# Kernel tuning notes

Measured on AMD Instinct MI355X. Metric: run time of the kernel, lower is better.

Reference implementation:

```python
import jax, jax.numpy as jnp
import numpy as np

D_MODEL = 1024
D_INNER = 4096   # expand=4
D_STATE = 16
D_CONV = 4
DT_RANK = 64     # ceil(d_model/16)
BATCH = 2
SEQLEN = 2048


def setup_inputs() -> dict:
    key = jax.random.key(0)
    ks = jax.random.split(key, 9)
    s = 0.02
    x = jax.random.normal(ks[0], (BATCH, SEQLEN, D_MODEL), jnp.float32)
    in_proj_w = jax.random.normal(ks[1], (D_MODEL, 2 * D_INNER), jnp.float32) * s
    conv_w = jax.random.normal(ks[2], (D_INNER, D_CONV), jnp.float32) * 0.3
    conv_b = jax.random.normal(ks[3], (D_INNER,), jnp.float32) * 0.02
    x_proj_w = jax.random.normal(ks[4], (D_INNER, DT_RANK + 2 * D_STATE), jnp.float32) * s
    dt_proj_w = jax.random.normal(ks[5], (DT_RANK, D_INNER), jnp.float32) * (DT_RANK ** -0.5)
    dt_proj_b = jax.random.normal(ks[6], (D_INNER,), jnp.float32) * 0.1 - 4.0  # small softplus(dt)
    # A = repeat(arange(1, d_state+1)) as in mamba-ssm; A_log = log(A)
    A_log = jnp.log(jnp.broadcast_to(jnp.arange(1, D_STATE + 1, dtype=jnp.float32), (D_INNER, D_STATE)))
    D = jnp.ones((D_INNER,), jnp.float32)
    out_proj_w = jax.random.normal(ks[7], (D_INNER, D_MODEL), jnp.float32) * s
    return {"x": x, "in_proj_w": in_proj_w, "conv_w": conv_w, "conv_b": conv_b,
            "x_proj_w": x_proj_w, "dt_proj_w": dt_proj_w, "dt_proj_b": dt_proj_b,
            "A_log": A_log, "D": D, "out_proj_w": out_proj_w}


def reference(x, in_proj_w, conv_w, conv_b, x_proj_w, dt_proj_w, dt_proj_b, A_log, D, out_proj_w):
    Bsz, L, _ = x.shape
    # input projection -> (x branch, gate z), each [B, L, d_inner]
    xz = x @ in_proj_w
    xc, z = jnp.split(xz, 2, axis=-1)
    # causal depthwise conv1d, kernel D_CONV, left-padded
    xp = jnp.pad(xc, ((0, 0), (D_CONV - 1, 0), (0, 0)))
    xconv = conv_b + sum(xp[:, k:k + L, :] * conv_w[:, k] for k in range(D_CONV))
    xs = jax.nn.silu(xconv)  # [B, L, d_inner]
    # input-dependent SSM params
    proj = xs @ x_proj_w  # [B, L, dt_rank + 2*d_state]
    dt_lo, Bt, Ct = jnp.split(proj, [DT_RANK, DT_RANK + D_STATE], axis=-1)
    dt = jax.nn.softplus(dt_lo @ dt_proj_w + dt_proj_b)  # [B, L, d_inner]
    A = -jnp.exp(A_log)  # [d_inner, d_state]

    def step(h, inp):
        dt_t, B_t, C_t, u_t = inp  # [B,dI], [B,dS], [B,dS], [B,dI]
        dA = jnp.exp(dt_t[..., None] * A)                       # [B, dI, dS]
        h = h * dA + (dt_t * u_t)[..., None] * B_t[:, None, :]  # [B, dI, dS]
        y = jnp.einsum('bdn,bn->bd', h, C_t)                    # [B, dI]
        return h, y

    h0 = jnp.zeros((Bsz, D_INNER, D_STATE), x.dtype)
    inps = (dt.transpose(1, 0, 2), Bt.transpose(1, 0, 2),
            Ct.transpose(1, 0, 2), xs.transpose(1, 0, 2))
    _, ys = jax.lax.scan(step, h0, inps)  # ys: [L, B, d_inner]
    y = ys.transpose(1, 0, 2) + xs * D
    y = y * jax.nn.silu(z)
    return y @ out_proj_w
```

## Files before the change

### kernel.cpp

```cpp
#include <hip/hip_runtime.h>
#include <hip/hip_bf16.h>

#define D_MODEL 1024
#define D_INNER 4096
#define D_STATE 16
#define D_CONV 4
#define DT_RANK 64
#define BATCH 2
#define SEQLEN 2048
#define MROWS (BATCH * SEQLEN)
#define NPROJ (DT_RANK + 2 * D_STATE)
#define PST 128
#define NC 32
#define TC (SEQLEN / NC)
#define KSPLIT 8
#define KSP6 4

typedef unsigned short u16;
typedef unsigned int u32;
typedef __attribute__((ext_vector_type(8))) short short8;
typedef __attribute__((ext_vector_type(4))) float floatx4;

#define LOG2E 1.44269504089f

__device__ __forceinline__ float bf2f(u16 u) {
    union { u32 i; float f; } v; v.i = ((u32)u) << 16; return v.f;
}
__device__ __forceinline__ u16 f2bf(float f) {
    union { float f; u32 i; } v; v.f = f;
    u32 x = v.i;
    u32 r = x + 0x7fffu + ((x >> 16) & 1u);
    return (u16)(r >> 16);
}
__device__ __forceinline__ float softplus_fast(float x) {
    float l = __logf(1.f + __expf(-fabsf(x)));
    return x > 0.f ? x + l : l;
}
__device__ __forceinline__ float sigmoid_fast(float x) {
    return __builtin_amdgcn_rcpf(1.f + __expf(-x));
}
__device__ __forceinline__ float exp2_hw(float x) {
    float r;
    asm("v_exp_f32 %0, %1" : "=v"(r) : "v"(x));
    return r;
}
__device__ __forceinline__ void pow_tree16(float r, float* pw) {
    pw[0] = r;
    pw[1] = r * r;
    pw[2] = pw[1] * r;
    pw[3] = pw[1] * pw[1];
    pw[4] = pw[3] * r;
    pw[5] = pw[3] * pw[1];
    pw[6] = pw[3] * pw[2];
    pw[7] = pw[3] * pw[3];
#pragma unroll
    for (int k = 0; k < 8; k++) pw[8 + k] = pw[7] * pw[k];
}
__device__ __forceinline__ void async_cp16(const u16* g, u16* l) {
    __builtin_amdgcn_global_load_lds((const __attribute__((address_space(1))) void*)g,
                                     (__attribute__((address_space(3))) void*)l, 16, 0, 0);
}

__global__ __launch_bounds__(256) void detect_dtype(const u16* __restrict__ x, int* __restrict__ flag,
                                                    int* __restrict__ sflag) {
    __shared__ int cnt;
    if (threadIdx.x == 0) { cnt = 0; *sflag = 0; }
    __syncthreads();
    int local = 0;
    for (int k = 0; k < 16; k++) {
        int e = threadIdx.x * 8192 + k * 512;
        u16 v = x[2 * e];
        int ex = (v >> 7) & 0xFF;
        if (ex >= 0x68 && ex <= 0x8F) local++;
    }
    atomicAdd(&cnt, local);
    __syncthreads();
    if (threadIdx.x == 0) *flag = (cnt >= 2458) ? 1 : 0;
}

__global__ __launch_bounds__(256) void ingest16(const void* __restrict__ src, u16* __restrict__ dst,
                                                int n, const int* __restrict__ flag) {
    int i = blockIdx.x * 256 + threadIdx.x;
    if (i >= n) return;
    if (*flag) dst[i] = ((const u16*)src)[i];
    else       dst[i] = f2bf(((const float*)src)[i]);
}

__global__ __launch_bounds__(256) void prep_small(const void* __restrict__ cw, const void* __restrict__ cb,
                                                  const void* __restrict__ dtb, const void* __restrict__ Dv,
                                                  const void* __restrict__ Alog,
                                                  u16* __restrict__ cw16, u16* __restrict__ cb16,
                                                  u16* __restrict__ dtb16, u16* __restrict__ D16,
                                                  float* __restrict__ A, const int* __restrict__ flag,
                                                  int* __restrict__ sflag) {
    int i = blockIdx.x * 256 + threadIdx.x;
    int isb = *flag;
    if (i < D_INNER * D_CONV)
        cw16[i] = isb ? ((const u16*)cw)[i] : f2bf(((const float*)cw)[i]);
    if (i < D_INNER) {
        cb16[i]  = isb ? ((const u16*)cb)[i]  : f2bf(((const float*)cb)[i]);
        dtb16[i] = isb ? ((const u16*)dtb)[i] : f2bf(((const float*)dtb)[i]);
        D16[i]   = isb ? ((const u16*)Dv)[i]  : f2bf(((const float*)Dv)[i]);
    }
    if (i < D_INNER * D_STATE) {
        float v = isb ? bf2f(((const u16*)Alog)[i]) : ((const float*)Alog)[i];
        float a = -expf(v);
        A[i] = a;
        float tgt = (float)((i & 15) + 1);
        if (fabsf(a + tgt) > 4e-6f * tgt) atomicOr(sflag, 1);
    }
}

__global__ __launch_bounds__(256) void transpose_w(const void* __restrict__ W, u16* __restrict__ WT,
                                                   int K, int N, const int* __restrict__ flag) {
    __shared__ float t[32][33];
    int k0 = blockIdx.y * 32, n0 = blockIdx.x * 32;
    int tid = threadIdx.x;
    int r = tid >> 3, c4 = (tid & 7) * 4;
    int isb = *flag;
    size_t base = (size_t)(k0 + r) * N + n0 + c4;
    float4 v;
    if (isb) { ushort4 u4 = *(const ushort4*)((const u16*)W + base);
               v = make_float4(bf2f(u4.x), bf2f(u4.y), bf2f(u4.z), bf2f(u4.w)); }
    else     { v = *(const float4*)((const float*)W + base); }
    t[c4 + 0][r] = v.x; t[c4 + 1][r] = v.y; t[c4 + 2][r] = v.z; t[c4 + 3][r] = v.w;
    __syncthreads();
    u16* o = WT + (size_t)(n0 + r) * K + k0 + c4;
    o[0] = f2bf(t[r][c4 + 0]);
    o[1] = f2bf(t[r][c4 + 1]);
    o[2] = f2bf(t[r][c4 + 2]);
    o[3] = f2bf(t[r][c4 + 3]);
}

template<int KS, int MODE>
__global__ __launch_bounds__(512, 2) void gemm8p(const u16* __restrict__ A, const u16* __restrict__ Bt,
                                                 u16* __restrict__ o0, u16* __restrict__ o1,
                                                 float* __restrict__ Pp) {
    __shared__ __align__(16) u16 lds[65536];
    const int tid = threadIdx.x;
    const int lane = tid & 63;
    const int wave = tid >> 6;
    const int wr = wave >> 2, wc = wave & 3;
    const int quad = lane >> 4, l15 = lane & 15;

    int m0, n0, kbase, kz;
    if (MODE == 0) {
        int wgid = (blockIdx.x & 7) * 64 + (blockIdx.x >> 3);
        m0 = (wgid & 15) * 256;
        n0 = (wgid >> 4) * 256;
        kbase = 0; kz = 0;
    } else {
        m0 = blockIdx.y * 256;
        n0 = blockIdx.x * 256;
        kz = blockIdx.z;
        kbase = kz * 1024;
    }
    const int NT = 1024 / 64;

    const int srow = tid >> 3;
    const int kswz = (((tid & 7) ^ (srow & 7)) << 3);
    const u16* pA = A + (size_t)(m0 + srow) * KS + kbase + kswz;
    const u16* pB = Bt + (size_t)(n0 + srow) * KS + kbase + kswz;

    const int rsw = (l15 & 7) << 3;
    const int ksel0 = (quad * 8) ^ rsw;
    const int ksel1 = (32 + quad * 8) ^ rsw;
    const int aoff = (wr * 64 + l15) * 64;
    const int boff = (wc * 32 + l15) * 64;

    floatx4 acc[8][4];
#pragma unroll
    for (int i = 0; i < 8; i++)
#pragma unroll
        for (int j = 0; j < 4; j++) acc[i][j] = (floatx4)0.f;
    short8 af[4][2];
    short8 bfr[2][2][2];

#define STAGE_A(nb, h, kt) do { \
    const u16* g_ = pA + (size_t)(h) * 128 * KS + (kt) * 64; \
    u16* l_ = &lds[((nb) * 2 + (h)) * 8192 + tid * 8]; \
    async_cp16(g_, l_); \
    async_cp16(g_ + (size_t)64 * KS, l_ + 4096); \
} while (0)
#define STAGE_B(nb, h, kt) do { \
    const u16* g_ = pB + (size_t)(h) * 128 * KS + (kt) * 64; \
    u16* l_ = &lds[32768 + ((nb) * 2 + (h)) * 8192 + tid * 8]; \
    async_cp16(g_, l_); \
    async_cp16(g_ + (size_t)64 * KS, l_ + 4096); \
} while (0)
#define LOADA(b, h) do { \
    const u16* p_ = &lds[((b) * 2 + (h)) * 8192 + aoff]; \
    _Pragma("unroll") \
    for (int ii = 0; ii < 4; ii++) { \
        af[ii][0] = *(const short8*)(p_ + ii * 1024 + ksel0); \
        af[ii][1] = *(const short8*)(p_ + ii * 1024 + ksel1); \
    } \
} while (0)
#define LOADB(b, h) do { \
    const u16* p_ = &lds[32768 + ((b) * 2 + (h)) * 8192 + boff]; \
    _Pragma("unroll") \
    for (int jj = 0; jj < 2; jj++) { \
        bfr[h][jj][0] = *(const short8*)(p_ + jj * 1024 + ksel0); \
        bfr[h][jj][1] = *(const short8*)(p_ + jj * 1024 + ksel1); \
    } \
} while (0)
#define MFMAQ(qa, qb) do { \
    __builtin_amdgcn_s_setprio(1); \
    _Pragma("unroll") \
    for (int ii = 0; ii < 4; ii++) \
    _Pragma("unroll") \
    for (int jj = 0; jj < 2; jj++) { \
        floatx4 c_ = acc[(qa) * 4 + ii][(qb) * 2 + jj]; \
        c_ = __builtin_amdgcn_mfma_f32_16x16x32_bf16(af[ii][0], bfr[qb][jj][0], c_, 0, 0, 0); \
        c_ = __builtin_amdgcn_mfma_f32_16x16x32_bf16(af[ii][1], bfr[qb][jj][1], c_, 0, 0, 0); \
        acc[(qa) * 4 + ii][(qb) * 2 + jj] = c_; \
    } \
    __builtin_amdgcn_s_setprio(0); \
} while (0)
#define VMW(N) asm volatile("s_waitcnt vmcnt(" #N ")" ::: "memory")
#define BARX() do { __builtin_amdgcn_s_barrier(); asm volatile("" ::: "memory"); } while (0)
#define SANDWICH() do { \
    __builtin_amdgcn_sched_barrier(0); \
    __builtin_amdgcn_s_barrier(); \
    asm volatile("s_waitcnt lgkmcnt(0)" ::: "memory"); \
    __builtin_amdgcn_sched_barrier(0); \
} while (0)

    STAGE_A(0, 0, 0);
    STAGE_B(0, 0, 0);
    STAGE_B(0, 1, 0);
    STAGE_A(0, 1, 0);
    VMW(4); BARX();

    for (int t = 0; t < NT - 1; ++t) {
        const int b = t & 1, nb = b ^ 1;
        LOADA(b, 0);
        LOADB(b, 0);
        STAGE_A(nb, 0, t + 1);
        SANDWICH();
        MFMAQ(0, 0);
        VMW(4); BARX();
        LOADB(b, 1);
        STAGE_B(nb, 0, t + 1);
        SANDWICH();
        MFMAQ(0, 1);
        VMW(4); BARX();
        LOADA(b, 1);
        STAGE_B(nb, 1, t + 1);
        SANDWICH();
        MFMAQ(1, 1);
        STAGE_A(nb, 1, t + 1);
        MFMAQ(1, 0);
        VMW(4); BARX();
    }
    {
        const int b = (NT - 1) & 1;
        LOADA(b, 0);
        LOADB(b, 0);
        SANDWICH();
        MFMAQ(0, 0);
        VMW(2); BARX();
        LOADB(b, 1);
        SANDWICH();
        MFMAQ(0, 1);
        VMW(0); BARX();
        LOADA(b, 1);
        MFMAQ(1, 1);
        MFMAQ(1, 0);
    }

    if constexpr (MODE == 0) {
        (void)kz; (void)Pp;
        u16* d = (n0 < D_INNER) ? o0 : o1;
        const int nb0 = (n0 < D_INNER) ? n0 : n0 - D_INNER;
        asm volatile("s_waitcnt lgkmcnt(0)" ::: "memory");
        BARX();
        u16* wbase = &lds[wave * 4608];
#pragma unroll
        for (int p = 0; p < 2; p++) {
#pragma unroll
            for (int i = 0; i < 4; i++) {
                const int lro = i * 16 + quad * 4;
#pragma unroll
                for (int j = 0; j < 4; j++) {
                    const int lc = (j >> 1) * 32 + (j & 1) * 16 + l15;
#pragma unroll
                    for (int r = 0; r < 4; r++)
                        wbase[(lro + r) * 72 + lc] = f2bf(acc[p * 4 + i][j][r]);
                }
            }
            asm volatile("s_waitcnt lgkmcnt(0)" ::: "memory");
            __builtin_amdgcn_sched_barrier(0);
            const int gr = m0 + p * 128 + wr * 64 + lane;
#pragma unroll
            for (int c = 0; c < 2; c++) {
                const u16* src = &wbase[lane * 72 + c * 32];
                u16* dst = &d[(size_t)gr * D_INNER + nb0 + c * 128 + wc * 32];
#pragma unroll
                for (int q = 0; q < 4; q++) {
                    short8 v = *(const short8*)(src + q * 8);
                    *(short8*)(dst + q * 8) = v;
                }
            }
            asm volatile("s_waitcnt lgkmcnt(0)" ::: "memory");
            __builtin_amdgcn_sched_barrier(0);
        }
    } else {
        (void)o0; (void)o1;
        float* d = Pp + (size_t)kz * MROWS * D_MODEL;
#pragma unroll
        for (int i = 0; i < 8; i++) {
            const int mrow = m0 + wr * 64 + (i & 3) * 16 + (i >> 2) * 128 + quad * 4;
#pragma unroll
            for (int j = 0; j < 4; j++) {
                const int ncol = n0 + wc * 32 + (j & 1) * 16 + (j >> 1) * 128 + l15;
#pragma unroll
                for (int r = 0; r < 4; r++)
                    d[(size_t)(mrow + r) * D_MODEL + ncol] = acc[i][j][r];
            }
        }
    }
#undef STAGE_A
#undef STAGE_B
#undef LOADA
#undef LOADB
#undef MFMAQ
#undef VMW
#undef BARX
#undef SANDWICH
}

__global__ __launch_bounds__(256) void reduce_out(const float* __restrict__ Pp, void* __restrict__ out,
                                                  const int* __restrict__ flag) {
    int i = (blockIdx.x * 256 + threadIdx.x) * 4;
    float4 s = *(const float4*)&Pp[i];
#pragma unroll
    for (int z = 1; z < KSP6; z++) {
        float4 p = *(const float4*)&Pp[(size_t)z * MROWS * D_MODEL + i];
        s.x += p.x; s.y += p.y; s.z += p.z; s.w += p.w;
    }
    if (*flag) {
        ushort4 o = make_ushort4(f2bf(s.x), f2bf(s.y), f2bf(s.z), f2bf(s.w));
        *(ushort4*)((u16*)out + i) = o;
    } else {
        *(float4*)((float*)out + i) = s;
    }
}

__global__ __launch_bounds__(256) void gemm_proj(const u16* __restrict__ A, const u16* __restrict__ Bt,
                                                 float* __restrict__ Pp) {
    const int K = D_INNER;
    __shared__ __align__(16) u16 sA[128 * 32];
    __shared__ __align__(16) u16 sB[128 * 32];
    int tid = threadIdx.x;
    int lane = tid & 63;
    int wave = tid >> 6;
    int wm = (wave >> 1) * 64, wn = (wave & 1) * 64;
    int quad = lane >> 4, l15 = lane & 15;
    int m0 = blockIdx.y * 128;
    int kz = blockIdx.x;
    int kbase = kz * (K / KSPLIT);

    floatx4 acc[4][4];
#pragma unroll
    for (int i = 0; i < 4; i++)
#pragma unroll
        for (int j = 0; j < 4; j++) acc[i][j] = (floatx4)0.f;

    const u16* ga0 = A + (size_t)(m0 + (tid >> 2)) * K + (tid & 3) * 8;
    const u16* ga1 = A + (size_t)(m0 + 64 + (tid >> 2)) * K + (tid & 3) * 8;
    const u16* gb0 = Bt + (size_t)(tid >> 2) * K + (tid & 3) * 8;
    const u16* gb1 = Bt + (size_t)(64 + (tid >> 2)) * K + (tid & 3) * 8;
    u16* la0 = &sA[tid * 8];
    u16* la1 = &sA[(256 + tid) * 8];
    u16* lb0 = &sB[tid * 8];
    u16* lb1 = &sB[(256 + tid) * 8];

    for (int k0 = kbase; k0 < kbase + K / KSPLIT; k0 += 32) {
        async_cp16(ga0 + k0, la0);
        async_cp16(ga1 + k0, la1);
        async_cp16(gb0 + k0, lb0);
        async_cp16(gb1 + k0, lb1);
        __syncthreads();
        short8 af[4], bf[4];
#pragma unroll
        for (int i = 0; i < 4; i++) {
            af[i] = *(const short8*)&sA[(wm + i * 16 + l15) * 32 + quad * 8];
            bf[i] = *(const short8*)&sB[(wn + i * 16 + l15) * 32 + quad * 8];
        }
#pragma unroll
        for (int i = 0; i < 4; i++)
#pragma unroll
            for (int j = 0; j < 4; j++)
                acc[i][j] = __builtin_amdgcn_mfma_f32_16x16x32_bf16(af[i], bf[j], acc[i][j], 0, 0, 0);
        __syncthreads();
    }

    float* d = Pp + (size_t)kz * MROWS * PST;
#pragma unroll
    for (int i = 0; i < 4; i++)
#pragma unroll
        for (int j = 0; j < 4; j++)
#pragma unroll
            for (int r = 0; r < 4; r++) {
                int mm = m0 + wm + i * 16 + quad * 4 + r;
                int nn = wn + j * 16 + l15;
                d[(size_t)mm * PST + nn] = acc[i][j][r];
            }
}

__global__ __launch_bounds__(256) void reduce_proj(const float* __restrict__ Pp, float* __restrict__ proj,
                                                   u16* __restrict__ proj_lo) {
    int i = blockIdx.x * 256 + threadIdx.x;
    float s = 0.f;
#pragma unroll
    for (int z = 0; z < KSPLIT; z++) s += Pp[(size_t)z * MROWS * PST + i];
    proj[i] = s;
    int col = i & (PST - 1);
    if (col < DT_RANK) proj_lo[(size_t)(i >> 7) * DT_RANK + col] = f2bf(s);
}

__global__ __launch_bounds__(256) void gemm_dt(const u16* __restrict__ A, const u16* __restrict__ Bt,
                                               const u16* __restrict__ dtb, u16* __restrict__ dt) {
    const int K = DT_RANK;
    __shared__ __align__(16) u16 smem[64 * 132];
    u16* sA = smem;
    u16* sB = smem + 128 * 32;
    int tid = threadIdx.x;
    int lane = tid & 63;
    int wave = tid >> 6;
    int wm = (wave >> 1) * 64, wn = (wave & 1) * 64;
    int quad = lane >> 4, l15 = lane & 15;
    int m0 = blockIdx.y * 128, n0 = blockIdx.x * 128;

    floatx4 acc[4][4];
#pragma unroll
    for (int i = 0; i < 4; i++)
#pragma unroll
        for (int j = 0; j < 4; j++) acc[i][j] = (floatx4)0.f;

    const u16* ga0 = A + (size_t)(m0 + (tid >> 2)) * K + (tid & 3) * 8;
    const u16* ga1 = A + (size_t)(m0 + 64 + (tid >> 2)) * K + (tid & 3) * 8;
    const u16* gb0 = Bt + (size_t)(n0 + (tid >> 2)) * K + (tid & 3) * 8;
    const u16* gb1 = Bt + (size_t)(n0 + 64 + (tid >> 2)) * K + (tid & 3) * 8;
    u16* la0 = &sA[tid * 8];
    u16* la1 = &sA[(256 + tid) * 8];
    u16* lb0 = &sB[tid * 8];
    u16* lb1 = &sB[(256 + tid) * 8];

    for (int k0 = 0; k0 < K; k0 += 32) {
        async_cp16(ga0 + k0, la0);
        async_cp16(ga1 + k0, la1);
        async_cp16(gb0 + k0, lb0);
        async_cp16(gb1 + k0, lb1);
        __syncthreads();
        short8 af[4], bf[4];
#pragma unroll
        for (int i = 0; i < 4; i++) {
            af[i] = *(const short8*)&sA[(wm + i * 16 + l15) * 32 + quad * 8];
            bf[i] = *(const short8*)&sB[(wn + i * 16 + l15) * 32 + quad * 8];
        }
#pragma unroll
        for (int i = 0; i < 4; i++)
#pragma unroll
            for (int j = 0; j < 4; j++)
                acc[i][j] = __builtin_amdgcn_mfma_f32_16x16x32_bf16(af[i], bf[j], acc[i][j], 0, 0, 0);
        __syncthreads();
    }

#pragma unroll
    for (int h = 0; h < 2; h++) {
        __syncthreads();
        if (wm == h * 64) {
#pragma unroll
            for (int j = 0; j < 4; j++) {
                int col = wn + j * 16 + l15;
                float b = bf2f(dtb[n0 + col]);
#pragma unroll
                for (int i = 0; i < 4; i++)
#pragma unroll
                    for (int r = 0; r < 4; r++) {
                        int row = i * 16 + quad * 4 + r;
                        smem[row * 132 + col] = f2bf(softplus_fast(acc[i][j][r] + b));
                    }
            }
        }
        __syncthreads();
#pragma unroll
        for (int p = 0; p < 4; p++) {
            int row = p * 16 + (tid >> 4);
            int chunk = tid & 15;
            uint4 v = *(const uint4*)&smem[row * 132 + chunk * 8];
            *(uint4*)&dt[(size_t)(m0 + h * 64 + row) * D_INNER + n0 + chunk * 8] = v;
        }
    }
}

__global__ __launch_bounds__(256) void conv_silu(const u16* __restrict__ xc, const u16* __restrict__ cw,
                                                 const u16* __restrict__ cb, u16* __restrict__ xs) {
    int idx = blockIdx.x * 256 + threadIdx.x;
    int g = idx & (D_INNER / 8 - 1);
    int bt = idx >> 9;
    int t = bt & (SEQLEN - 1);
    int d0 = g * 8;
    size_t row = (size_t)bt * D_INNER + d0;
    u16 wv[32];
    *(uint4*)&wv[0]  = *(const uint4*)&cw[d0 * 4];
    *(uint4*)&wv[8]  = *(const uint4*)&cw[d0 * 4 + 8];
    *(uint4*)&wv[16] = *(const uint4*)&cw[d0 * 4 + 16];
    *(uint4*)&wv[24] = *(const uint4*)&cw[d0 * 4 + 24];
    u16 cbv[8];
    *(uint4*)&cbv[0] = *(const uint4*)&cb[d0];
    u16 x0[8] = {0, 0, 0, 0, 0, 0, 0, 0};
    u16 x1[8] = {0, 0, 0, 0, 0, 0, 0, 0};
    u16 x2[8] = {0, 0, 0, 0, 0, 0, 0, 0};
    u16 x3[8];
    if (t >= 3) *(uint4*)x0 = *(const uint4*)&xc[row - 3 * (size_t)D_INNER];
    if (t >= 2) *(uint4*)x1 = *(const uint4*)&xc[row - 2 * (size_t)D_INNER];
    if (t >= 1) *(uint4*)x2 = *(const uint4*)&xc[row - 1 * (size_t)D_INNER];
    *(uint4*)x3 = *(const uint4*)&xc[row];
    u16 out[8];
#pragma unroll
    for (int ch = 0; ch < 8; ch++) {
        float a = bf2f(cbv[ch]);
        a += bf2f(x0[ch]) * bf2f(wv[ch * 4 + 0]);
        a += bf2f(x1[ch]) * bf2f(wv[ch * 4 + 1]);
        a += bf2f(x2[ch]) * bf2f(wv[ch * 4 + 2]);
        a += bf2f(x3[ch]) * bf2f(wv[ch * 4 + 3]);
        out[ch] = f2bf(a * sigmoid_fast(a));
    }
    *(uint4*)&xs[row] = *(const uint4*)&out[0];
}

__global__ __launch_bounds__(256) void scan_phase1(const float* __restrict__ proj, const u16* __restrict__ dt,
                                                   const float* __restrict__ A, const u16* __restrict__ xs,
                                                   float* __restrict__ hloc, float* __restrict__ Ssum,
                                                   const int* __restrict__ sflag) {
    int d = blockIdx.x * 256 + threadIdx.x;
    int c = blockIdx.y, b = blockIdx.z;
    int t0 = c * TC;
    int structured = (*sflag == 0);
    float h[16];
#pragma unroll
    for (int n = 0; n < 16; n++) h[n] = 0.f;
    float S = 0.f;
    size_t base = ((size_t)b * SEQLEN + t0) * D_INNER + d;
    const float* prow = proj + ((size_t)b * SEQLEN + t0) * PST + DT_RANK;
    u16 dcur = dt[base], ucur = xs[base];
    if (structured) {
        for (int t = 0; t < TC; t++) {
            size_t nidx = base + (size_t)((t + 1 < TC) ? t + 1 : t) * D_INNER;
            u16 dnxt = dt[nidx];
            u16 unxt = xs[nidx];
            float4 B0 = *(const float4*)(prow + t * PST + 0);
            float4 B1 = *(const float4*)(prow + t * PST + 4);
            float4 B2 = *(const float4*)(prow + t * PST + 8);
            float4 B3 = *(const float4*)(prow + t * PST + 12);
            float dtv = bf2f(dcur), u = bf2f(ucur);
            S += dtv;
            float du = dtv * u;
            float Bf[16] = {B0.x, B0.y, B0.z, B0.w, B1.x, B1.y, B1.z, B1.w,
                            B2.x, B2.y, B2.z, B2.w, B3.x, B3.y, B3.z, B3.w};
            float pw[16];
            pow_tree16(exp2_hw(-LOG2E * dtv), pw);
#pragma unroll
            for (int n = 0; n < 16; n++)
                h[n] = h[n] * pw[n] + du * Bf[n];
            dcur = dnxt; ucur = unxt;
        }
    } else {
        float Areg[16];
        const float4* Ap = (const float4*)(A + (size_t)d * 16);
#pragma unroll
        for (int n = 0; n < 4; n++) {
            float4 v = Ap[n];
            Areg[n * 4 + 0] = v.x * LOG2E; Areg[n * 4 + 1] = v.y * LOG2E;
            Areg[n * 4 + 2] = v.z * LOG2E; Areg[n * 4 + 3] = v.w * LOG2E;
        }
        for (int t = 0; t < TC; t++) {
            size_t nidx = base + (size_t)((t + 1 < TC) ? t + 1 : t) * D_INNER;
            u16 dnxt = dt[nidx];
            u16 unxt = xs[nidx];
            float4 B0 = *(const float4*)(prow + t * PST + 0);
            float4 B1 = *(const float4*)(prow + t * PST + 4);
            float4 B2 = *(const float4*)(prow + t * PST + 8);
            float4 B3 = *(const float4*)(prow + t * PST + 12);
            float dtv = bf2f(dcur), u = bf2f(ucur);
            S += dtv;
            float du = dtv * u;
            float Bf[16] = {B0.x, B0.y, B0.z, B0.w, B1.x, B1.y, B1.z, B1.w,
                            B2.x, B2.y, B2.z, B2.w, B3.x, B3.y, B3.z, B3.w};
#pragma unroll
            for (int n = 0; n < 16; n++)
                h[n] = h[n] * exp2_hw(dtv * Areg[n]) + du * Bf[n];
            dcur = dnxt; ucur = unxt;
        }
    }
    float* hp = &hloc[(((size_t)b * NC + c) * D_INNER + d) * 16];
#pragma unroll
    for (int n = 0; n < 16; n += 4)
        *(float4*)&hp[n] = make_float4(h[n], h[n + 1], h[n + 2], h[n + 3]);
    Ssum[((size_t)b * NC + c) * D_INNER + d] = S;
}

__global__ __launch_bounds__(256) void scan_phase2(const float* __restrict__ A, const float* __restrict__ Ssum,
                                                   float* __restrict__ hloc) {
    int tid = blockIdx.x * 256 + threadIdx.x;
    int n = tid & 15;
    int d = (tid >> 4) & (D_INNER - 1);
    int b = tid >> 16;
    float An2 = A[d * 16 + n] * LOG2E;
    float h = 0.f;
    for (int c = 0; c < NC; c++) {
        size_t idx = (((size_t)b * NC + c) * D_INNER + d) * 16 + n;
        float hl = hloc[idx];
        float S = Ssum[((size_t)b * NC + c) * D_INNER + d];
        hloc[idx] = h;
        h = hl + h * exp2_hw(An2 * S);
    }
}

__global__ __launch_bounds__(256) void scan_phase3(const float* __restrict__ proj, const u16* __restrict__ dt,
                                                   const float* __restrict__ A, const u16* __restrict__ D16,
                                                   const float* __restrict__ hinit, const u16* __restrict__ z16,
                                                   u16* __restrict__ xs, const int* __restrict__ sflag) {
    int d = blockIdx.x * 256 + threadIdx.x;
    int c = blockIdx.y, b = blockIdx.z;
    int t0 = c * TC;
    int structured = (*sflag == 0);
    float h[16];
    {
        const float* hp = &hinit[(((size_t)b * NC + c) * D_INNER + d) * 16];
#pragma unroll
        for (int n = 0; n < 16; n += 4) {
            float4 v = *(const float4*)&hp[n];
            h[n] = v.x; h[n + 1] = v.y; h[n + 2] = v.z; h[n + 3] = v.w;
        }
    }
    float Dd = bf2f(D16[d]);
    size_t base = ((size_t)b * SEQLEN + t0) * D_INNER + d;
    const float* prow = proj + ((size_t)b * SEQLEN + t0) * PST + DT_RANK;
    u16 dcur = dt[base], ucur = xs[base], zcur = z16[base];
    if (structured) {
        for (int t = 0; t < TC; t++) {
            size_t nidx = base + (size_t)((t + 1 < TC) ? t + 1 : t) * D_INNER;
            u16 dnxt = dt[nidx];
            u16 unxt = xs[nidx];
            u16 znxt = z16[nidx];
            float4 B0 = *(const float4*)(prow + t * PST + 0);
            float4 B1 = *(const float4*)(prow + t * PST + 4);
            float4 B2 = *(const float4*)(prow + t * PST + 8);
            float4 B3 = *(const float4*)(prow + t * PST + 12);
            float4 C0 = *(const float4*)(prow + t * PST + 16);
            float4 C1 = *(const float4*)(prow + t * PST + 20);
            float4 C2 = *(const float4*)(prow + t * PST + 24);
            float4 C3 = *(const float4*)(prow + t * PST + 28);
            float dtv = bf2f(dcur), u = bf2f(ucur), zv = bf2f(zcur);
            float du = dtv * u;
            float Bf[16] = {B0.x, B0.y, B0.z, B0.w, B1.x, B1.y, B1.z, B1.w,
                            B2.x, B2.y, B2.z, B2.w, B3.x, B3.y, B3.z, B3.w};
            float Cf[16] = {C0.x, C0.y, C0.z, C0.w, C1.x, C1.y, C1.z, C1.w,
                            C2.x, C2.y, C2.z, C2.w, C3.x, C3.y, C3.z, C3.w};
            float pw[16];
            pow_tree16(exp2_hw(-LOG2E * dtv), pw);
            float y = 0.f;
#pragma unroll
            for (int n = 0; n < 16; n++) {
                h[n] = h[n] * pw[n] + du * Bf[n];
                y += h[n] * Cf[n];
            }
            float gate = zv * sigmoid_fast(zv);
            xs[base + (size_t)t * D_INNER] = f2bf((y + u * Dd) * gate);
            dcur = dnxt; ucur = unxt; zcur = znxt;
        }
    } else {
        float Areg[16];
        const float4* Ap = (const float4*)(A + (size_t)d * 16);
#pragma unroll
        for (int n = 0; n < 4; n++) {
            float4 v = Ap[n];
            Areg[n * 4 + 0] = v.x * LOG2E; Areg[n * 4 + 1] = v.y * LOG2E;
            Areg[n * 4 + 2] = v.z * LOG2E; Areg[n * 4 + 3] = v.w * LOG2E;
        }
        for (int t = 0; t < TC; t++) {
            size_t nidx = base + (size_t)((t + 1 < TC) ? t + 1 : t) * D_INNER;
            u16 dnxt = dt[nidx];
            u16 unxt = xs[nidx];
            u16 znxt = z16[nidx];
            float4 B0 = *(const float4*)(prow + t * PST + 0);
            float4 B1 = *(const float4*)(prow + t * PST + 4);
            float4 B2 = *(const float4*)(prow + t * PST + 8);
            float4 B3 = *(const float4*)(prow + t * PST + 12);
            float4 C0 = *(const float4*)(prow + t * PST + 16);
            float4 C1 = *(const float4*)(prow + t * PST + 20);
            float4 C2 = *(const float4*)(prow + t * PST + 24);
            float4 C3 = *(const float4*)(prow + t * PST + 28);
            float dtv = bf2f(dcur), u = bf2f(ucur), zv = bf2f(zcur);
            float du = dtv * u;
            float Bf[16] = {B0.x, B0.y, B0.z, B0.w, B1.x, B1.y, B1.z, B1.w,
                            B2.x, B2.y, B2.z, B2.w, B3.x, B3.y, B3.z, B3.w};
            float Cf[16] = {C0.x, C0.y, C0.z, C0.w, C1.x, C1.y, C1.z, C1.w,
                            C2.x, C2.y, C2.z, C2.w, C3.x, C3.y, C3.z, C3.w};
            float y = 0.f;
#pragma unroll
            for (int n = 0; n < 16; n++) {
                h[n] = h[n] * exp2_hw(dtv * Areg[n]) + du * Bf[n];
                y += h[n] * Cf[n];
            }
            float gate = zv * sigmoid_fast(zv);
            xs[base + (size_t)t * D_INNER] = f2bf((y + u * Dd) * gate);
            dcur = dnxt; ucur = unxt; zcur = znxt;
        }
    }
}

extern "C" void kernel_launch(void* const* d_in, const int* in_sizes, int n_in,
                              void* d_out, int out_size, void* d_ws, size_t ws_size,
                              hipStream_t stream) {
    const void* x          = d_in[0];
    const void* in_proj_w  = d_in[1];
    const void* conv_w     = d_in[2];
    const void* conv_b     = d_in[3];
    const void* x_proj_w   = d_in[4];
    const void* dt_proj_w  = d_in[5];
    const void* dt_proj_b  = d_in[6];
    const void* A_log      = d_in[7];
    const void* Dvec       = d_in[8];
    const void* out_proj_w = d_in[9];

    char* w = (char*)d_ws;
    const size_t MB = 1024 * 1024;
    const size_t KB = 1024;
    int*   flag    = (int*)(w + 0);
    int*   sflag   = (int*)(w + 16);
    float* Aws     = (float*)(w + 1 * KB);
    float* proj    = (float*)(w + 1 * MB);
    u16*   cw16    = (u16*)(w + 3 * MB);
    u16*   cb16    = (u16*)(w + 3 * MB + 64 * KB);
    u16*   dtb16   = (u16*)(w + 3 * MB + 128 * KB);
    u16*   D16     = (u16*)(w + 3 * MB + 192 * KB);
    u16*   proj_lo = (u16*)(w + 3 * MB + 512 * KB);
    u16*   dtwT    = (u16*)(w + 4 * MB);
    u16*   buf1    = (u16*)(w + 5 * MB);
    u16*   dt16    = buf1;
    u16*   zbuf    = (u16*)(w + 37 * MB);
    float* Pp6     = (float*)(w + 5 * MB);
    u16*   xs      = (u16*)(w + 69 * MB);
    u16*   x16     = (u16*)(w + 101 * MB);
    u16*   ipwT    = (u16*)(w + 110 * MB);
    float* Pp      = (float*)(w + 101 * MB);
    float* hloc    = (float*)(w + 101 * MB);
    float* Ssum    = (float*)(w + 117 * MB);
    u16*   opwT    = (u16*)(w + 127 * MB);
    u16*   xpwT    = (u16*)(w + 136 * MB);

    detect_dtype<<<dim3(1), dim3(256), 0, stream>>>((const u16*)x, flag, sflag);
    prep_small<<<dim3(256), dim3(256), 0, stream>>>(conv_w, conv_b, dt_proj_b, Dvec, A_log,
                                                    cw16, cb16, dtb16, D16, Aws, flag, sflag);
    ingest16<<<dim3(MROWS * D_MODEL / 256), dim3(256), 0, stream>>>(x, x16, MROWS * D_MODEL, flag);
    transpose_w<<<dim3(2 * D_INNER / 32, D_MODEL / 32), dim3(256), 0, stream>>>(in_proj_w, ipwT, D_MODEL, 2 * D_INNER, flag);
    transpose_w<<<dim3(D_MODEL / 32, D_INNER / 32), dim3(256), 0, stream>>>(out_proj_w, opwT, D_INNER, D_MODEL, flag);
    transpose_w<<<dim3(NPROJ / 32, D_INNER / 32), dim3(256), 0, stream>>>(x_proj_w, xpwT, D_INNER, NPROJ, flag);
    transpose_w<<<dim3(D_INNER / 32, DT_RANK / 32), dim3(256), 0, stream>>>(dt_proj_w, dtwT, DT_RANK, D_INNER, flag);

    gemm8p<1024, 0><<<dim3(512), dim3(512), 0, stream>>>(x16, ipwT, buf1, zbuf, nullptr);
    conv_silu<<<dim3(MROWS * D_INNER / 8 / 256), dim3(256), 0, stream>>>(buf1, cw16, cb16, xs);
    gemm_proj<<<dim3(KSPLIT, MROWS / 128), dim3(256), 0, stream>>>(xs, xpwT, Pp);
    reduce_proj<<<dim3(MROWS * PST / 256), dim3(256), 0, stream>>>(Pp, proj, proj_lo);
    gemm_dt<<<dim3(D_INNER / 128, MROWS / 128), dim3(256), 0, stream>>>(proj_lo, dtwT, dtb16, dt16);
    scan_phase1<<<dim3(D_INNER / 256, NC, BATCH), dim3(256), 0, stream>>>(proj, dt16, Aws, xs, hloc, Ssum, sflag);
    scan_phase2<<<dim3(BATCH * D_INNER * D_STATE / 256), dim3(256), 0, stream>>>(Aws, Ssum, hloc);
    scan_phase3<<<dim3(D_INNER / 256, NC, BATCH), dim3(256), 0, stream>>>(proj, dt16, Aws, D16, hloc, zbuf, xs, sflag);
    gemm8p<4096, 1><<<dim3(D_MODEL / 256, MROWS / 256, KSP6), dim3(512), 0, stream>>>(xs, opwT, nullptr, nullptr, Pp6);
    reduce_out<<<dim3(MROWS * D_MODEL / 1024), dim3(256), 0, stream>>>(Pp6, d_out, flag);
}
```

Measured before the change: 438.3 us.

## Merge GEMM main-loop phases into two barriers and store bf16 epilogue directly

The GEMM main loop goes from three barrier-separated phases per K-tile to two. Fragment loads and next-tile staging are grouped ahead of larger MFMA blocks, and the vmcnt waits are adjusted to match. The MODE 0 epilogue now writes bf16 results straight from the accumulators to global memory instead of transposing through LDS for 16-byte stores. This cuts barrier and LDS round-trip overhead, but the global stores become scattered 2-byte writes and register pressure from the earlier fragment loads may rise.

```diff
diff --git a/kernel.cpp b/kernel.cpp
--- a/kernel.cpp
+++ b/kernel.cpp
@@ -225,46 +225,48 @@
     asm volatile("s_waitcnt lgkmcnt(0)" ::: "memory"); \
     __builtin_amdgcn_sched_barrier(0); \
 } while (0)
+#define LDRAIN() do { \
+    __builtin_amdgcn_sched_barrier(0); \
+    asm volatile("s_waitcnt lgkmcnt(0)" ::: "memory"); \
+    __builtin_amdgcn_sched_barrier(0); \
+} while (0)
 
     STAGE_A(0, 0, 0);
     STAGE_B(0, 0, 0);
     STAGE_B(0, 1, 0);
     STAGE_A(0, 1, 0);
-    VMW(4); BARX();
+    VMW(2); BARX();
 
     for (int t = 0; t < NT - 1; ++t) {
         const int b = t & 1, nb = b ^ 1;
         LOADA(b, 0);
         LOADB(b, 0);
+        LOADB(b, 1);
         STAGE_A(nb, 0, t + 1);
+        STAGE_B(nb, 0, t + 1);
         SANDWICH();
         MFMAQ(0, 0);
-        VMW(4); BARX();
-        LOADB(b, 1);
-        STAGE_B(nb, 0, t + 1);
-        SANDWICH();
         MFMAQ(0, 1);
         VMW(4); BARX();
         LOADA(b, 1);
         STAGE_B(nb, 1, t + 1);
+        STAGE_A(nb, 1, t + 1);
         SANDWICH();
         MFMAQ(1, 1);
-        STAGE_A(nb, 1, t + 1);
         MFMAQ(1, 0);
-        VMW(4); BARX();
+        VMW(2); BARX();
     }
     {
         const int b = (NT - 1) & 1;
         LOADA(b, 0);
         LOADB(b, 0);
+        LOADB(b, 1);
         SANDWICH();
         MFMAQ(0, 0);
-        VMW(2); BARX();
-        LOADB(b, 1);
-        SANDWICH();
         MFMAQ(0, 1);
         VMW(0); BARX();
         LOADA(b, 1);
+        LDRAIN();
         MFMAQ(1, 1);
         MFMAQ(1, 0);
     }
@@ -273,37 +275,16 @@
         (void)kz; (void)Pp;
         u16* d = (n0 < D_INNER) ? o0 : o1;
         const int nb0 = (n0 < D_INNER) ? n0 : n0 - D_INNER;
-        asm volatile("s_waitcnt lgkmcnt(0)" ::: "memory");
-        BARX();
-        u16* wbase = &lds[wave * 4608];
-#pragma unroll
-        for (int p = 0; p < 2; p++) {
-#pragma unroll
-            for (int i = 0; i < 4; i++) {
-                const int lro = i * 16 + quad * 4;
-#pragma unroll
-                for (int j = 0; j < 4; j++) {
-                    const int lc = (j >> 1) * 32 + (j & 1) * 16 + l15;
-#pragma unroll
-                    for (int r = 0; r < 4; r++)
-                        wbase[(lro + r) * 72 + lc] = f2bf(acc[p * 4 + i][j][r]);
-                }
+#pragma unroll
+        for (int i = 0; i < 8; i++) {
+            const int mrow = m0 + wr * 64 + (i & 3) * 16 + (i >> 2) * 128 + quad * 4;
+#pragma unroll
+            for (int j = 0; j < 4; j++) {
+                const int ncol = nb0 + wc * 32 + (j & 1) * 16 + (j >> 1) * 128 + l15;
+#pragma unroll
+                for (int r = 0; r < 4; r++)
+                    d[(size_t)(mrow + r) * D_INNER + ncol] = f2bf(acc[i][j][r]);
             }
-            asm volatile("s_waitcnt lgkmcnt(0)" ::: "memory");
-            __builtin_amdgcn_sched_barrier(0);
-            const int gr = m0 + p * 128 + wr * 64 + lane;
-#pragma unroll
-            for (int c = 0; c < 2; c++) {
-                const u16* src = &wbase[lane * 72 + c * 32];
-                u16* dst = &d[(size_t)gr * D_INNER + nb0 + c * 128 + wc * 32];
-#pragma unroll
-                for (int q = 0; q < 4; q++) {
-                    short8 v = *(const short8*)(src + q * 8);
-                    *(short8*)(dst + q * 8) = v;
-                }
-            }
-            asm volatile("s_waitcnt lgkmcnt(0)" ::: "memory");
-            __builtin_amdgcn_sched_barrier(0);
         }
     } else {
         (void)o0; (void)o1;
@@ -328,6 +309,7 @@
 #undef VMW
 #undef BARX
 #undef SANDWICH
+#undef LDRAIN
 }
 
 __global__ __launch_bounds__(256) void reduce_out(const float* __restrict__ Pp, void* __restrict__ out,
```

After: 430.4 us. No clear change (-1.8%).
